# Performance work log

Measured on AMD Instinct MI355X. Metric: run time of the kernel, lower is better.

The kernel has to match this reference:

```python
import jax, jax.numpy as jnp
from jax import lax
import numpy as np

PERCENTAGES = [0.004, 0.006, 0.008, 0.01, 0.012]
RADIUS = 1.0  # shape == 'square'
B, N = 4, 8192


def setup_inputs() -> dict:
    key = jax.random.key(0)
    adv_pcs = jax.random.uniform(key, (B, N, 3), dtype=jnp.float32)
    return {"adv_pcs": adv_pcs}


def _gather_points(pcs, idx):
    # pcs [B,N,3], idx [B,S] -> [B,S,3]
    idx3 = jnp.broadcast_to(idx[:, :, None], idx.shape + (3,))
    return jnp.take_along_axis(pcs, idx3, axis=1)


def farthest_point_sample(pcs, n_samples):
    # iterative FPS starting at index 0; returns indices [B, n_samples]
    Bb, Nn, _ = pcs.shape

    def step(carry, _):
        min_d2, last = carry  # [B,N], [B]
        p = _gather_points(pcs, last[:, None])  # [B,1,3]
        d2 = jnp.sum((pcs - p) ** 2, axis=-1)  # [B,N]
        min_d2 = jnp.minimum(min_d2, d2)
        nxt = jnp.argmax(min_d2, axis=-1).astype(jnp.int32)
        return (min_d2, nxt), last

    init = (jnp.full((Bb, Nn), 1e10, pcs.dtype), jnp.zeros((Bb,), jnp.int32))
    _, idx = lax.scan(step, init, None, length=n_samples)
    return jnp.transpose(idx)  # [B, n_samples]


def ball_query(seeds, pcs, r, K):
    # seeds [B,S,3], pcs [B,N,3] -> pts [B,S,K,3], idx [B,S,K] (-1 padded)
    d2 = jnp.sum((seeds[:, :, None, :] - pcs[:, None, :, :]) ** 2, axis=-1)  # [B,S,N]
    valid = d2 < r * r
    # stable sort: in-radius points first, preserving index order
    order = jnp.argsort(jnp.where(valid, 0, 1).astype(jnp.int32), axis=-1, stable=True)
    idx = order[..., :K]  # [B,S,K]
    cnt = jnp.sum(valid, axis=-1)  # [B,S]
    keep = jnp.arange(K)[None, None, :] < cnt[:, :, None]
    idx = jnp.where(keep, idx, -1)
    pts = jax.vmap(lambda p, i: p[i])(pcs, jnp.clip(idx, 0))  # [B,S,K,3]
    return pts, idx


def knn_second_sqdist(groups, lengths):
    # groups [G,K,3]; first `lengths[g]` rows of each group are valid candidates.
    # Returns squared distance to the 2nd nearest neighbor (incl. self at 0) [G,K].
    G, K, _ = groups.shape
    d2 = jnp.sum((groups[:, :, None, :] - groups[:, None, :, :]) ** 2, axis=-1)  # [G,K,K]
    col_ok = jnp.arange(K)[None, None, :] < lengths[:, None, None]
    d2 = jnp.where(col_ok, d2, jnp.inf)
    top2 = -lax.top_k(-d2, 2)[0]  # two smallest along candidates
    nn2 = top2[:, :, 1]  # second smallest (first is self, dist 0)
    return jnp.where(jnp.isfinite(nn2), nn2, 0.0)  # pad like pytorch3d (0 for missing)


def reference(adv_pcs):
    Bb, Nn, _ = adv_pcs.shape
    dt = adv_pcs.dtype
    seed_num = int(Nn * 0.05)
    fps_idx = farthest_point_sample(adv_pcs, seed_num)
    seeds = _gather_points(adv_pcs, fps_idx)  # [B,seed,3]
    loss = jnp.zeros((Bb,), dt)
    for p in PERCENTAGES:
        exp_num = Nn * p
        r = float(np.sqrt(p) * RADIUS)
        expect_dis = jnp.sqrt(jnp.asarray(np.pi * RADIUS ** 2 / exp_num * p, dt))
        K = int(2 * exp_num)
        pts, idx = ball_query(seeds, adv_pcs, r, K)
        pts = pts.reshape(Bb * seed_num, K, 3)
        idx = idx.reshape(Bb * seed_num, K)
        mask = idx != -1  # [G,K]
        gnum = jnp.sum(mask, axis=-1)  # [G], >= 1 (seed itself in-radius)
        nn2 = knn_second_sqdist(pts, gnum)  # [G,K] squared dists
        safe = jnp.where(nn2 > 0, nn2, 1.0)
        nn_dis = jnp.where(nn2 > 0, jnp.sqrt(safe), 0.0)
        clutter = jnp.square(nn_dis - expect_dis) / (expect_dis + 1e-12)
        # faithful to torch: sum over ALL elements, then elementwise divide by counts
        clutter_vec = jnp.sum(clutter * mask) / gnum.astype(dt)  # [G]
        imbalance = jnp.square(gnum.astype(dt) - exp_num) / exp_num  # [G]
        ul = (clutter_vec * imbalance).reshape(Bb, seed_num).mean(axis=-1)  # [B]
        loss = loss + ul
    return loss / len(PERCENTAGES)
```

## Files before the change

### kernel.cpp

```cpp
#include <hip/hip_runtime.h>
#include <math.h>

#define N_PTS 8192
#define B_SZ 4
#define SEED_NUM 409
#define FPS_THREADS 256
#define LTOT 653
#define N_GROUPS (B_SZ * SEED_NUM)

typedef float f2 __attribute__((ext_vector_type(2)));
typedef float f4 __attribute__((ext_vector_type(4)));

__device__ __forceinline__ float sqdist(float ax, float ay, float az,
                                        float bx, float by, float bz) {
  float dx = __fsub_rn(ax, bx);
  float dy = __fsub_rn(ay, by);
  float dz = __fsub_rn(az, bz);
  return __fadd_rn(__fadd_rn(__fmul_rn(dx, dx), __fmul_rn(dy, dy)),
                   __fmul_rn(dz, dz));
}

#define FOR16(M) \
  M(0) M(1) M(2) M(3) M(4) M(5) M(6) M(7) \
  M(8) M(9) M(10) M(11) M(12) M(13) M(14) M(15)

template <int CTRL>
__device__ __forceinline__ unsigned long long dpp_u64_bc1(
    unsigned long long k) {
  const unsigned lo2 = (unsigned)__builtin_amdgcn_update_dpp(
      0, (int)(unsigned)k, CTRL, 0xf, 0xf, true);
  const unsigned hi2 = (unsigned)__builtin_amdgcn_update_dpp(
      0, (int)(unsigned)(k >> 32), CTRL, 0xf, 0xf, true);
  return ((unsigned long long)hi2 << 32) | lo2;
}
template <int CTRL, int ROW_MASK>
__device__ __forceinline__ unsigned long long dpp_u64_keep(
    unsigned long long k) {
  const unsigned lo2 = (unsigned)__builtin_amdgcn_update_dpp(
      (int)(unsigned)k, (int)(unsigned)k, CTRL, ROW_MASK, 0xf, false);
  const unsigned hi2 = (unsigned)__builtin_amdgcn_update_dpp(
      (int)(unsigned)(k >> 32), (int)(unsigned)(k >> 32), CTRL, ROW_MASK, 0xf,
      false);
  return ((unsigned long long)hi2 << 32) | lo2;
}

__global__ __launch_bounds__(FPS_THREADS, 1) void fps_kernel(
    const float* __restrict__ pcs, float* __restrict__ seeds,
    double* __restrict__ sums ) {
#pragma clang fp contract(off)
  const int b = blockIdx.x;
  const int tid = threadIdx.x;
  const int lane = tid & 63, wid = tid >> 6;
  const float* base = pcs + (size_t)b * N_PTS * 3;

  if (b == 0 && tid < 26) sums[tid] = 0.0;

  __shared__ f4 spts4[N_PTS];
  __shared__ float seedbuf[SEED_NUM * 3];
  __shared__ __align__(16) unsigned long long red[2][4];

#define FPS_DECL(j) f2 px##j, py##j, pz##j, md##j;
  FOR16(FPS_DECL)
#undef FPS_DECL

#define FPS_INIT(j)                                   \
  {                                                   \
    const int i0 = tid + (2 * (j)) * FPS_THREADS;     \
    const int i1 = i0 + FPS_THREADS;                  \
    px##j = (f2){base[i0 * 3 + 0], base[i1 * 3 + 0]}; \
    py##j = (f2){base[i0 * 3 + 1], base[i1 * 3 + 1]}; \
    pz##j = (f2){base[i0 * 3 + 2], base[i1 * 3 + 2]}; \
    md##j = (f2){1e10f, 1e10f};   \
    spts4[i0] = (f4){px##j.x, py##j.x, pz##j.x, 0.f}; \
    spts4[i1] = (f4){px##j.y, py##j.y, pz##j.y, 0.f}; \
  }
  FOR16(FPS_INIT)
#undef FPS_INIT

#define FPS_PIN(j) asm volatile("" : "+v"(px##j), "+v"(py##j), "+v"(pz##j));
  FOR16(FPS_PIN)
#undef FPS_PIN

  float cx = base[0], cy = base[1], cz = base[2];

  for (int s = 0; s < SEED_NUM; ++s) {
    if (tid == 0) {
      seedbuf[s * 3 + 0] = cx;
      seedbuf[s * 3 + 1] = cy;
      seedbuf[s * 3 + 2] = cz;
    }
    const f2 ccx = (f2){cx, cx}, ccy = (f2){cy, cy}, ccz = (f2){cz, cz};
    float bv = -1.0f;
    int bi = 0;
#define FPS_UPD(j)                                                      \
  {                                                                     \
    const f2 dx = px##j - ccx;                                          \
    const f2 dy = py##j - ccy;                                          \
    const f2 dz = pz##j - ccz;                                          \
    const f2 t0 = dx * dx;                                              \
    const f2 t1 = dy * dy;                                              \
    const f2 t2 = dz * dz;                                              \
    const f2 d2 = (t0 + t1) + t2;                                       \
    const f2 m = __builtin_elementwise_min(md##j, d2);                  \
    md##j = m;                                                          \
    if (m.x > bv) { bv = m.x; bi = tid + (2 * (j)) * FPS_THREADS; }     \
    if (m.y > bv) { bv = m.y; bi = tid + (2 * (j) + 1) * FPS_THREADS; } \
  }
    FOR16(FPS_UPD)
#undef FPS_UPD
    unsigned long long key =
        ((unsigned long long)__float_as_uint(bv) << 32) |
        (unsigned long long)(unsigned)(N_PTS - 1 - bi);
    unsigned long long o;
    o = dpp_u64_bc1<0x111>(key);         key = (o > key) ? o : key;
    o = dpp_u64_bc1<0x112>(key);         key = (o > key) ? o : key;
    o = dpp_u64_bc1<0x114>(key);         key = (o > key) ? o : key;
    o = dpp_u64_bc1<0x118>(key);         key = (o > key) ? o : key;
    o = dpp_u64_keep<0x142, 0xa>(key);   key = (o > key) ? o : key;
    o = dpp_u64_keep<0x143, 0xc>(key);   key = (o > key) ? o : key;
    if (lane == 63) red[s & 1][wid] = key;
    __syncthreads();
    const ulonglong2* rp = (const ulonglong2*)(&red[s & 1][0]);
    const ulonglong2 r01 = rp[0];
    const ulonglong2 r23 = rp[1];
    const unsigned long long ka = (r01.y > r01.x) ? r01.y : r01.x;
    const unsigned long long kb = (r23.y > r23.x) ? r23.y : r23.x;
    const unsigned long long kmax = (kb > ka) ? kb : ka;
    const int ci = N_PTS - 1 - (int)(unsigned)(kmax & 0xffffffffull);
    const f4 c = spts4[ci];
    cx = c.x;
    cy = c.y;
    cz = c.z;
  }

  __syncthreads();
  float* sg = seeds + (size_t)b * SEED_NUM * 3;
  for (int i = tid; i < SEED_NUM * 3; i += FPS_THREADS) sg[i] = seedbuf[i];
}

__global__ __launch_bounds__(256) void group_kernel(
    const float* __restrict__ pcs, const float* __restrict__ seeds,
    double* __restrict__ totS , double* __restrict__ accA ,
    unsigned int* __restrict__ dcnt, float* __restrict__ out) {
  const int g = blockIdx.x;
  const int b = g / SEED_NUM;
  const int tid = threadIdx.x;
  const int lane = tid & 63, wid = tid >> 6;

  const int Kc[5] = {65, 98, 131, 163, 196};
  const int off[5] = {0, 65, 163, 294, 457};
  const double Pd[5] = {0.004, 0.006, 0.008, 0.01, 0.012};
  float r2c[5], expnf[5], expdc[5];
#pragma unroll
  for (int p = 0; p < 5; ++p) {
    const double pd = Pd[p];
    const double rd = sqrt(pd);
    r2c[p] = (float)(rd * rd);
    const double expn_d = 8192.0 * pd;
    expnf[p] = (float)expn_d;
    expdc[p] = sqrtf((float)(M_PI / expn_d * pd));
  }

  const float* base = pcs + (size_t)b * N_PTS * 3;
  const float* sp = seeds + (size_t)g * 3;
  const float sx = sp[0], sy = sp[1], sz = sp[2];

  __shared__ f4 lpt[LTOT];
  __shared__ int cnt[5];
  __shared__ int wtot[4];
  __shared__ double wsum[5][4];
  __shared__ int islast;

  if (tid < 5) cnt[tid] = 0;
  __syncthreads();

  const float r2max = r2c[4];
  for (int i = tid; i < N_PTS; i += 256) {
    const float x = base[i * 3 + 0];
    const float y = base[i * 3 + 1];
    const float z = base[i * 3 + 2];
    const float d2 = sqdist(x, y, z, sx, sy, sz);
    if (d2 < r2max) {
#pragma unroll
      for (int p = 0; p < 5; ++p) {
        if (d2 < r2c[p]) {
          const int pos = atomicAdd(&cnt[p], 1);
          if (pos < Kc[p]) {
            lpt[off[p] + pos] = (f4){x, y, z, 0.f};
          }
        }
      }
    }
  }
  __syncthreads();

#pragma unroll
  for (int p = 0; p < 5; ++p) {
    if (cnt[p] > Kc[p]) {
      int run = 0;
      for (int base_i = 0; base_i < N_PTS; base_i += 256) {
        const int i = base_i + tid;
        const float x = base[i * 3 + 0];
        const float y = base[i * 3 + 1];
        const float z = base[i * 3 + 2];
        const float d2 = sqdist(x, y, z, sx, sy, sz);
        const bool valid = d2 < r2c[p];
        const unsigned long long m = __ballot(valid);
        if (lane == 0) wtot[wid] = __popcll(m);
        __syncthreads();
        int pos = run + __popcll(m & ((1ull << lane) - 1ull));
        for (int w = 0; w < wid; ++w) pos += wtot[w];
        if (valid && pos < Kc[p]) {
          lpt[off[p] + pos] = (f4){x, y, z, 0.f};
        }
        run += wtot[0] + wtot[1] + wtot[2] + wtot[3];
        __syncthreads();
      }
    }
  }

#pragma unroll
  for (int p = 0; p < 5; ++p) {
    const int gn = min(cnt[p], Kc[p]);
    const float ed = expdc[p];
    const int lb = off[p];
    double localS = 0.0;
    for (int r0 = 0; r0 < gn; r0 += 64) {
      const int row = r0 + (tid >> 2);
      const int sub = tid & 3;
      float m1 = INFINITY, m2 = INFINITY;
      if (row < gn) {
        const f4 pi = lpt[lb + row];
        for (int j = sub; j < gn; j += 4) {
          const f4 pj = lpt[lb + j];
          const float d2 = sqdist(pi.x, pi.y, pi.z, pj.x, pj.y, pj.z);
          if (d2 < m1) { m2 = m1; m1 = d2; }
          else if (d2 < m2) { m2 = d2; }
        }
      }
#pragma unroll
      for (int d = 1; d <= 2; d <<= 1) {
        const float om1 = __shfl_xor(m1, d);
        const float om2 = __shfl_xor(m2, d);
        const float lo = fminf(m1, om1);
        const float hi = fmaxf(m1, om1);
        m2 = fminf(fminf(m2, om2), hi);
        m1 = lo;
      }
      if (row < gn && sub == 0) {
        const float nn2 = (m2 > 1e37f) ? 0.0f : m2;
        const float nnd = (nn2 > 0.0f) ? sqrtf(nn2) : 0.0f;
        const float diff = __fsub_rn(nnd, ed);
        const float clut = __fdiv_rn(__fmul_rn(diff, diff),
                                     __fadd_rn(ed, 1e-12f));
        localS += (double)clut;
      }
    }
#pragma unroll
    for (int o = 32; o > 0; o >>= 1) localS += __shfl_down(localS, o);
    if (lane == 0) wsum[p][wid] = localS;
  }
  __syncthreads();

  if (tid < 5) {
    const double S = wsum[tid][0] + wsum[tid][1] + wsum[tid][2] + wsum[tid][3];
    atomicAdd(&totS[tid], S);
  } else if (tid < 10) {
    const int p = tid - 5;
    const int gn = min(cnt[p], Kc[p]);
    const float gf = (float)gn;
    const float dd = __fsub_rn(gf, expnf[p]);
    const float imb = __fdiv_rn(__fmul_rn(dd, dd), expnf[p]);
    atomicAdd(&accA[p * 4 + b], (double)imb / (double)gf);
  }

  __syncthreads();
  if (tid == 0) {
    __threadfence();
    const unsigned int old = atomicAdd(dcnt, 1u);
    islast = (old == (unsigned int)(N_GROUPS - 1)) ? 1 : 0;
  }
  __syncthreads();
  if (islast) {
    __shared__ double fin[25];
    if (tid < 25) {
      const double* src = (tid < 5) ? &totS[tid] : &accA[tid - 5];
      fin[tid] = atomicAdd((double*)src, 0.0);
    }
    __syncthreads();
    if (tid < B_SZ) {
      double acc = 0.0;
#pragma unroll
      for (int p = 0; p < 5; ++p)
        acc += fin[p] * (fin[5 + p * 4 + tid] / (double)SEED_NUM);
      out[tid] = (float)(acc / 5.0);
    }
  }
}

extern "C" void kernel_launch(void* const* d_in, const int* in_sizes, int n_in,
                              void* d_out, int out_size, void* d_ws,
                              size_t ws_size, hipStream_t stream) {
  (void)in_sizes; (void)n_in; (void)out_size; (void)ws_size;
  const float* pcs = (const float*)d_in[0];
  float* out = (float*)d_out;

  float* seeds = (float*)d_ws;
  double* sums = (double*)((char*)d_ws + 19632);

  fps_kernel<<<B_SZ, FPS_THREADS, 0, stream>>>(pcs, seeds, sums);
  group_kernel<<<N_GROUPS, 256, 0, stream>>>(
      pcs, seeds, sums, sums + 5, (unsigned int*)(sums + 25), out);
}
```

Before: 438.0 us.

## Store ball points once sorted by radius tier and share kNN scans across radii

After: 433.0 us. About the same (-1.1%).

```diff
diff --git a/kernel.cpp b/kernel.cpp
--- a/kernel.cpp
+++ b/kernel.cpp
@@ -57,7 +57,7 @@
 
   __shared__ f4 spts4[N_PTS];
   __shared__ float seedbuf[SEED_NUM * 3];
-  __shared__ __align__(16) unsigned long long red[2][4];
+  __shared__ unsigned long long red[2][4];
 
 #define FPS_DECL(j) f2 px##j, py##j, pz##j, md##j;
   FOR16(FPS_DECL)
@@ -120,12 +120,12 @@
     o = dpp_u64_keep<0x143, 0xc>(key);   key = (o > key) ? o : key;
     if (lane == 63) red[s & 1][wid] = key;
     __syncthreads();
-    const ulonglong2* rp = (const ulonglong2*)(&red[s & 1][0]);
-    const ulonglong2 r01 = rp[0];
-    const ulonglong2 r23 = rp[1];
-    const unsigned long long ka = (r01.y > r01.x) ? r01.y : r01.x;
-    const unsigned long long kb = (r23.y > r23.x) ? r23.y : r23.x;
-    const unsigned long long kmax = (kb > ka) ? kb : ka;
+    unsigned long long kmax = red[s & 1][0];
+#pragma unroll
+    for (int w = 1; w < 4; ++w) {
+      const unsigned long long t = red[s & 1][w];
+      kmax = (t > kmax) ? t : kmax;
+    }
     const int ci = N_PTS - 1 - (int)(unsigned)(kmax & 0xffffffffull);
     const f4 c = spts4[ci];
     cx = c.x;
@@ -165,38 +165,127 @@
   const float* sp = seeds + (size_t)g * 3;
   const float sx = sp[0], sy = sp[1], sz = sp[2];
 
+  __shared__ f4 tmp[LTOT];
   __shared__ f4 lpt[LTOT];
-  __shared__ int cnt[5];
+  __shared__ int tcnt[5], tbase[5], bcnt[5], ccum[5];
+  __shared__ int ntmp, capped;
   __shared__ int wtot[4];
   __shared__ double wsum[5][4];
   __shared__ int islast;
 
-  if (tid < 5) cnt[tid] = 0;
+  if (tid < 5) { tcnt[tid] = 0; bcnt[tid] = 0; }
+  if (tid == 0) ntmp = 0;
   __syncthreads();
 
   const float r2max = r2c[4];
-  for (int i = tid; i < N_PTS; i += 256) {
-    const float x = base[i * 3 + 0];
-    const float y = base[i * 3 + 1];
-    const float z = base[i * 3 + 2];
-    const float d2 = sqdist(x, y, z, sx, sy, sz);
-    if (d2 < r2max) {
-#pragma unroll
-      for (int p = 0; p < 5; ++p) {
-        if (d2 < r2c[p]) {
-          const int pos = atomicAdd(&cnt[p], 1);
-          if (pos < Kc[p]) {
-            lpt[off[p] + pos] = (f4){x, y, z, 0.f};
-          }
-        }
-      }
-    }
-  }
-  __syncthreads();
-
-#pragma unroll
-  for (int p = 0; p < 5; ++p) {
-    if (cnt[p] > Kc[p]) {
+  const f4* base4 = (const f4*)base;
+#define PROC(X, Y, Z)                                                       \
+  {                                                                         \
+    const float d2 = sqdist((X), (Y), (Z), sx, sy, sz);                     \
+    if (d2 < r2max) {                                                       \
+      const int tier = (d2 < r2c[0]) ? 0                                    \
+                       : (d2 < r2c[1]) ? 1                                  \
+                       : (d2 < r2c[2]) ? 2                                  \
+                       : (d2 < r2c[3]) ? 3 : 4;                             \
+      atomicAdd(&tcnt[tier], 1);                                            \
+      const int pos = atomicAdd(&ntmp, 1);                                  \
+      if (pos < LTOT) tmp[pos] = (f4){(X), (Y), (Z), (float)tier};          \
+    }                                                                       \
+  }
+  for (int it = 0; it < 8; ++it) {
+    const int q = it * 256 + tid;
+    const f4 v0 = base4[q * 3 + 0];
+    const f4 v1 = base4[q * 3 + 1];
+    const f4 v2 = base4[q * 3 + 2];
+    PROC(v0.x, v0.y, v0.z)
+    PROC(v0.w, v1.x, v1.y)
+    PROC(v1.z, v1.w, v2.x)
+    PROC(v2.y, v2.z, v2.w)
+  }
+#undef PROC
+  __syncthreads();
+
+  if (tid == 0) {
+    int acc = 0, cap = 0;
+#pragma unroll
+    for (int t = 0; t < 5; ++t) {
+      tbase[t] = acc;
+      acc += tcnt[t];
+      ccum[t] = acc;
+    }
+#pragma unroll
+    for (int p = 0; p < 5; ++p) cap |= (ccum[p] > Kc[p]) ? 1 : 0;
+    capped = cap;
+  }
+  __syncthreads();
+
+  const int nt = min(ntmp, LTOT);
+  for (int t = tid; t < nt; t += 256) {
+    const f4 e = tmp[t];
+    const int tier = (int)e.w;
+    const int pos = tbase[tier] + atomicAdd(&bcnt[tier], 1);
+    if (pos < LTOT) lpt[pos] = (f4){e.x, e.y, e.z, 0.f};
+  }
+  __syncthreads();
+
+  if (!capped) {
+    const int c0 = ccum[0], c1 = ccum[1], c2 = ccum[2], c3 = ccum[3],
+              c4 = ccum[4];
+    double lS0 = 0.0, lS1 = 0.0, lS2 = 0.0, lS3 = 0.0, lS4 = 0.0;
+    for (int r0 = 0; r0 < c4; r0 += 64) {
+      const int row = r0 + (tid >> 2);
+      const int sub = tid & 3;
+      const bool rok = row < c4;
+      const f4 pi = lpt[rok ? row : 0];
+      float m1 = INFINITY, m2 = INFINITY;
+      int j = sub;
+#define SEGMENT(CP, EDP, LSP)                                               \
+  {                                                                         \
+    for (; j < (CP); j += 4) {                                              \
+      const f4 pj = lpt[j];                                                 \
+      const float d2 = sqdist(pi.x, pi.y, pi.z, pj.x, pj.y, pj.z);          \
+      if (d2 < m1) { m2 = m1; m1 = d2; }                                    \
+      else if (d2 < m2) { m2 = d2; }                                        \
+    }                                                                       \
+        \
+    float s1 = m1, s2 = m2;                                                 \
+    {                                                                       \
+      const float o1 = __shfl_xor(s1, 1), o2 = __shfl_xor(s2, 1);           \
+      const float lo = fminf(s1, o1), hi = fmaxf(s1, o1);                   \
+      s2 = fminf(fminf(s2, o2), hi); s1 = lo;                               \
+    }                                                                       \
+    {                                                                       \
+      const float o1 = __shfl_xor(s1, 2), o2 = __shfl_xor(s2, 2);           \
+      const float lo = fminf(s1, o1), hi = fmaxf(s1, o1);                   \
+      s2 = fminf(fminf(s2, o2), hi); s1 = lo;                               \
+    }                                                                       \
+    if (rok && sub == 0 && row < (CP)) {                                    \
+      const float nn2 = (s2 > 1e37f) ? 0.0f : s2;             \
+      const float nnd = (nn2 > 0.0f) ? sqrtf(nn2) : 0.0f;                   \
+      const float diff = __fsub_rn(nnd, (EDP));                             \
+      const float clut = __fdiv_rn(__fmul_rn(diff, diff),                   \
+                                   __fadd_rn((EDP), 1e-12f));               \
+      LSP += (double)clut;                                                  \
+    }                                                                       \
+  }
+      SEGMENT(c0, expdc[0], lS0)
+      SEGMENT(c1, expdc[1], lS1)
+      SEGMENT(c2, expdc[2], lS2)
+      SEGMENT(c3, expdc[3], lS3)
+      SEGMENT(c4, expdc[4], lS4)
+#undef SEGMENT
+    }
+#define RED(LSP, P)                                          \
+  {                                                          \
+    double v = (LSP);                                        \
+    for (int o = 32; o > 0; o >>= 1) v += __shfl_down(v, o); \
+    if (lane == 0) wsum[(P)][wid] = v;                       \
+  }
+    RED(lS0, 0) RED(lS1, 1) RED(lS2, 2) RED(lS3, 3) RED(lS4, 4)
+#undef RED
+  } else {
+#pragma unroll
+    for (int p = 0; p < 5; ++p) {
       int run = 0;
       for (int base_i = 0; base_i < N_PTS; base_i += 256) {
         const int i = base_i + tid;
@@ -217,48 +306,48 @@
         __syncthreads();
       }
     }
-  }
-
-#pragma unroll
-  for (int p = 0; p < 5; ++p) {
-    const int gn = min(cnt[p], Kc[p]);
-    const float ed = expdc[p];
-    const int lb = off[p];
-    double localS = 0.0;
-    for (int r0 = 0; r0 < gn; r0 += 64) {
-      const int row = r0 + (tid >> 2);
-      const int sub = tid & 3;
-      float m1 = INFINITY, m2 = INFINITY;
-      if (row < gn) {
-        const f4 pi = lpt[lb + row];
-        for (int j = sub; j < gn; j += 4) {
-          const f4 pj = lpt[lb + j];
-          const float d2 = sqdist(pi.x, pi.y, pi.z, pj.x, pj.y, pj.z);
-          if (d2 < m1) { m2 = m1; m1 = d2; }
-          else if (d2 < m2) { m2 = d2; }
+#pragma unroll
+    for (int p = 0; p < 5; ++p) {
+      const int gn = min(ccum[p], Kc[p]);
+      const float ed = expdc[p];
+      const int lb = off[p];
+      double localS = 0.0;
+      for (int r0 = 0; r0 < gn; r0 += 64) {
+        const int row = r0 + (tid >> 2);
+        const int sub = tid & 3;
+        float m1 = INFINITY, m2 = INFINITY;
+        if (row < gn) {
+          const f4 pi = lpt[lb + row];
+          for (int j = sub; j < gn; j += 4) {
+            const f4 pj = lpt[lb + j];
+            const float d2 = sqdist(pi.x, pi.y, pi.z, pj.x, pj.y, pj.z);
+            if (d2 < m1) { m2 = m1; m1 = d2; }
+            else if (d2 < m2) { m2 = d2; }
+          }
+        }
+#pragma unroll
+        for (int d = 1; d <= 2; d <<= 1) {
+          const float om1 = __shfl_xor(m1, d);
+          const float om2 = __shfl_xor(m2, d);
+          const float lo = fminf(m1, om1);
+          const float hi = fmaxf(m1, om1);
+          m2 = fminf(fminf(m2, om2), hi);
+          m1 = lo;
+        }
+        if (row < gn && sub == 0) {
+          const float nn2 = (m2 > 1e37f) ? 0.0f : m2;
+          const float nnd = (nn2 > 0.0f) ? sqrtf(nn2) : 0.0f;
+          const float diff = __fsub_rn(nnd, ed);
+          const float clut = __fdiv_rn(__fmul_rn(diff, diff),
+                                       __fadd_rn(ed, 1e-12f));
+          localS += (double)clut;
         }
       }
 #pragma unroll
-      for (int d = 1; d <= 2; d <<= 1) {
-        const float om1 = __shfl_xor(m1, d);
-        const float om2 = __shfl_xor(m2, d);
-        const float lo = fminf(m1, om1);
-        const float hi = fmaxf(m1, om1);
-        m2 = fminf(fminf(m2, om2), hi);
-        m1 = lo;
-      }
-      if (row < gn && sub == 0) {
-        const float nn2 = (m2 > 1e37f) ? 0.0f : m2;
-        const float nnd = (nn2 > 0.0f) ? sqrtf(nn2) : 0.0f;
-        const float diff = __fsub_rn(nnd, ed);
-        const float clut = __fdiv_rn(__fmul_rn(diff, diff),
-                                     __fadd_rn(ed, 1e-12f));
-        localS += (double)clut;
-      }
-    }
-#pragma unroll
-    for (int o = 32; o > 0; o >>= 1) localS += __shfl_down(localS, o);
-    if (lane == 0) wsum[p][wid] = localS;
+      for (int o = 32; o > 0; o >>= 1) localS += __shfl_down(localS, o);
+      if (lane == 0) wsum[p][wid] = localS;
+      __syncthreads();
+    }
   }
   __syncthreads();
 
@@ -267,7 +356,7 @@
     atomicAdd(&totS[tid], S);
   } else if (tid < 10) {
     const int p = tid - 5;
-    const int gn = min(cnt[p], Kc[p]);
+    const int gn = min(ccum[p], Kc[p]);
     const float gf = (float)gn;
     const float dd = __fsub_rn(gf, expnf[p]);
     const float imb = __fdiv_rn(__fmul_rn(dd, dd), expnf[p]);
```
